# Optimization experiments

Hardware: AMD Instinct MI355X
Metric: run time of the kernel (lower is better)

Reference implementation:

```python
import jax, jax.numpy as jnp
import numpy as np

B_SZ, SEQ_LEN, STATE_DIM, D_IN, D_OUT, KX = 8, 2048, 1024, 512, 512, 10


def setup_inputs() -> dict:
    key = jax.random.key(0)
    ks = jax.random.split(key, 7)
    inputs = jax.random.normal(ks[0], (B_SZ, SEQ_LEN, D_IN), dtype=jnp.float32)
    h0 = jax.random.normal(ks[1], (STATE_DIM,), dtype=jnp.float32)
    # exponential_decay_init(lam=15): x = clamp(-1/lam * log(1-u), max=1); A = (1-x)*sign
    u = jax.random.uniform(ks[2], (STATE_DIM,), dtype=jnp.float32)
    x = jnp.minimum(-(1.0 / 15.0) * jnp.log1p(-u), 1.0)
    sign = jnp.sign(jax.random.normal(ks[3], (STATE_DIM,), dtype=jnp.float32))
    A = (1.0 - x) * sign
    Bm = jax.random.normal(ks[4], (D_IN, STATE_DIM), dtype=jnp.float32) / D_IN
    C = jax.random.normal(ks[5], (STATE_DIM, D_OUT), dtype=jnp.float32) / STATE_DIM
    M = jax.random.normal(ks[6], (D_OUT, D_IN, KX), dtype=jnp.float32) / D_OUT
    return {"inputs": inputs, "h0": h0, "A": A, "B": Bm, "C": C, "M": M}


def _ar_preds(M, x):
    # Equivalent to einsum('oik,bli->bklo') + per-k roll + triu mask + sum over k:
    # ar[b,l,:] = sum_{i=0}^{k-1, i<=l} M[:,:,i] @ x[b, l-i, :]
    b, l, d_in = x.shape
    kx = M.shape[2]
    ar = jnp.einsum('oi,bli->blo', M[:, :, 0], x)
    for i in range(1, kx):
        x_shift = jnp.pad(x, ((0, 0), (i, 0), (0, 0)))[:, :l]  # shift right, zero-fill
        ar = ar + jnp.einsum('oi,bli->blo', M[:, :, i], x_shift)
    return ar


def reference(inputs, h0, A, B, C, M):
    b, l, d_in = inputs.shape
    state_dim = A.shape[0]
    # Project inputs once: u_t @ B for all t -> [b, l, s]
    uB = jnp.einsum('bli,is->bls', inputs, B)

    def step(h, u_t):
        h = A * h + u_t  # diagonal recurrence
        return h, h

    h_init = jnp.broadcast_to(h0, (b, state_dim))
    _, hs = jax.lax.scan(step, h_init, jnp.swapaxes(uB, 0, 1))  # [l, b, s]
    hs = jnp.swapaxes(hs, 0, 1)  # [b, l, s]
    lds_out = hs @ C  # [b, l, d_out]
    return lds_out + _ar_preds(M, inputs)
```

## Files before the change

### kernel.cpp

```cpp
#include <hip/hip_runtime.h>

#define B_SZ   8
#define SEQ    2048
#define PSEQ   (SEQ+16)
#define SDIM   1024
#define DIN    512
#define DOUT   512
#define KX     10
#define RTOT   (B_SZ*SEQ)
#define LC     64
#define NC     (SEQ/LC)

typedef __attribute__((ext_vector_type(8))) short short8;
typedef __attribute__((ext_vector_type(4))) float f32x4;
typedef __attribute__((ext_vector_type(4))) unsigned short bfx4;

#define OFF_XP   0UL
#define OFF_UB   16973824UL
#define OFF_HS   50528256UL
#define OFF_BT   84082688UL
#define OFF_CT   85131264UL
#define OFF_MT   86179840UL

__device__ __forceinline__ short f2bf(float f) {
  unsigned u = __builtin_bit_cast(unsigned, f);
  u += 0x7fffu + ((u >> 16) & 1u);
  return (short)(u >> 16);
}
__device__ __forceinline__ float bf2f(unsigned short b) {
  return __builtin_bit_cast(float, (unsigned)b << 16);
}

#define GLOAD16(gp, lp) __builtin_amdgcn_global_load_lds( \
    (const __attribute__((address_space(1))) void*)(gp), \
    (__attribute__((address_space(3))) void*)(lp), 16, 0, 0)
#define WAITVM(n) asm volatile("s_waitcnt vmcnt(" #n ")" ::: "memory")
#define LGKM0()   do { asm volatile("s_waitcnt lgkmcnt(0)" ::: "memory"); \
                       __builtin_amdgcn_sched_barrier(0); } while (0)
#define SBAR() __builtin_amdgcn_s_barrier()

struct Frags { short8 a[4][2]; short8 b[4][2]; };

__device__ __forceinline__ void read_frags(Frags& f, const short* la, int aoff,
                                           const short* lb, int lane, int wm, int wn) {
  int lr = lane & 15, h = lane >> 4;
  #pragma unroll
  for (int kk = 0; kk < 2; ++kk) {
    int kslot = kk * 4 + h;
    #pragma unroll
    for (int mi = 0; mi < 4; ++mi) {
      int row = aoff + wm * 64 + mi * 16 + lr;
      f.a[mi][kk] = *reinterpret_cast<const short8*>(la + row * 64 + ((kslot ^ (row & 7)) << 3));
    }
    #pragma unroll
    for (int ni = 0; ni < 4; ++ni) {
      int row = wn * 64 + ni * 16 + lr;
      f.b[ni][kk] = *reinterpret_cast<const short8*>(lb + row * 64 + ((kslot ^ (row & 7)) << 3));
    }
  }
}

__device__ __forceinline__ void mfma_frags(const Frags& f, f32x4 acc[4][4]) {
  #pragma unroll
  for (int kk = 0; kk < 2; ++kk)
    #pragma unroll
    for (int mi = 0; mi < 4; ++mi)
      #pragma unroll
      for (int ni = 0; ni < 4; ++ni)
        acc[mi][ni] = __builtin_amdgcn_mfma_f32_16x16x32_bf16(f.a[mi][kk], f.b[ni][kk], acc[mi][ni], 0, 0, 0);
}

__device__ __forceinline__ void sgb_interleave() {
  #pragma unroll
  for (int i = 0; i < 16; ++i) {
    __builtin_amdgcn_sched_group_barrier(0x008, 2, 0);
    __builtin_amdgcn_sched_group_barrier(0x100, 1, 0);
  }
}

__device__ __forceinline__ void stageA256(const short* __restrict__ g, int ld,
                                          short* l, int tid) {
  int rsub = tid >> 3;
  int slot = (tid & 7) ^ (rsub & 7);
  #pragma unroll
  for (int i = 0; i < 4; ++i) {
    int row = i * 64 + rsub;
    GLOAD16(g + (size_t)row * ld + slot * 8, l + row * 64 + (tid & 7) * 8);
  }
}
__device__ __forceinline__ void stageB128(const short* __restrict__ g, int ld,
                                          short* l, int tid) {
  int rsub = tid >> 3;
  int slot = (tid & 7) ^ (rsub & 7);
  #pragma unroll
  for (int i = 0; i < 2; ++i) {
    int row = i * 64 + rsub;
    GLOAD16(g + (size_t)row * ld + slot * 8, l + row * 64 + (tid & 7) * 8);
  }
}
__device__ __forceinline__ void stageX320(const short* __restrict__ g,
                                          short* l, int tid) {
  int rsub = tid >> 3;
  int slot = (tid & 7) ^ (rsub & 7);
  #pragma unroll
  for (int i = 0; i < 5; ++i) {
    int row = i * 64 + rsub;
    GLOAD16(g + (size_t)row * DIN + slot * 8, l + row * 64 + (tid & 7) * 8);
  }
}

__global__ void k_prep1(const float* __restrict__ x, const float* __restrict__ B,
                        short* __restrict__ Xp, short* __restrict__ Bt) {
  __shared__ float t[32][33];
  int blk = blockIdx.x, tid = threadIdx.x;
  if (blk < 2048) {
    const int NG = RTOT * (DIN / 8);
    const int NPAD = B_SZ * 16 * (DIN / 8);
    for (int g = blk * 256 + tid; g < NG + NPAD; g += 2048 * 256) {
      if (g < NG) {
        int r = g >> 6, c8 = g & 63;
        int b = r >> 11, tt = r & 2047;
        const float4* p = reinterpret_cast<const float4*>(x) + (size_t)g * 2;
        float4 f0 = p[0], f1 = p[1];
        short8 o;
        o[0]=f2bf(f0.x); o[1]=f2bf(f0.y); o[2]=f2bf(f0.z); o[3]=f2bf(f0.w);
        o[4]=f2bf(f1.x); o[5]=f2bf(f1.y); o[6]=f2bf(f1.z); o[7]=f2bf(f1.w);
        *reinterpret_cast<short8*>(Xp + ((size_t)(b * PSEQ + 16 + tt) * DIN + c8 * 8)) = o;
      } else {
        int idx = g - NG;
        int b = idx >> 10, rem = idx & 1023;
        int row16 = rem >> 6, c8 = rem & 63;
        const short8 z = {0,0,0,0,0,0,0,0};
        *reinterpret_cast<short8*>(Xp + ((size_t)(b * PSEQ + row16) * DIN + c8 * 8)) = z;
      }
    }
  } else {
    int idx = blk - 2048;
    int bx = (idx & 31) * 32, by = (idx >> 5) * 32;
    int tx = tid & 31, ty = tid >> 5;
    #pragma unroll
    for (int j = 0; j < 32; j += 8)
      t[ty + j][tx] = B[(size_t)(by + ty + j) * SDIM + (bx + tx)];
    __syncthreads();
    #pragma unroll
    for (int j = 0; j < 32; j += 8)
      Bt[(size_t)(bx + ty + j) * DIN + (by + tx)] = f2bf(t[tx][ty + j]);
  }
}

__global__ void k_scan_h(const short* __restrict__ uB, const float* __restrict__ A,
                         const float* __restrict__ h0, const float* __restrict__ E,
                         short* __restrict__ hs,
                         const float* __restrict__ C, const float* __restrict__ M,
                         short* __restrict__ Ct, short* __restrict__ Mt) {
  __shared__ float t[32][33];
  int blk = blockIdx.x, tid = threadIdx.x;
  if (blk < 256) {
    int b = blk >> 5, c = blk & 31;
    int s0 = tid * 4;
    float a[4], h[4], ap[4];
    #pragma unroll
    for (int j = 0; j < 4; ++j) {
      a[j] = A[s0 + j];
      float p = a[j];
      #pragma unroll
      for (int q = 0; q < 6; ++q) p *= p;
      ap[j] = p;
      h[j] = h0[s0 + j];
    }
    const float* Eb = E + (size_t)b * NC * SDIM + s0;
    for (int c2 = 0; c2 < c; ++c2) {
      float4 ev = *reinterpret_cast<const float4*>(Eb + (size_t)c2 * SDIM);
      h[0] = fmaf(ap[0], h[0], ev.x);
      h[1] = fmaf(ap[1], h[1], ev.y);
      h[2] = fmaf(ap[2], h[2], ev.z);
      h[3] = fmaf(ap[3], h[3], ev.w);
    }
    const short* base = uB + ((size_t)b * SEQ + (size_t)c * LC) * SDIM + s0;
    short* hbase = hs + ((size_t)b * SEQ + (size_t)c * LC) * SDIM + s0;
    for (int tt = 0; tt < LC; ++tt) {
      bfx4 v = *reinterpret_cast<const bfx4*>(base + (size_t)tt * SDIM);
      bfx4 o;
      #pragma unroll
      for (int j = 0; j < 4; ++j) {
        h[j] = fmaf(a[j], h[j], bf2f(v[j]));
        o[j] = (unsigned short)f2bf(h[j]);
      }
      *reinterpret_cast<bfx4*>(hbase + (size_t)tt * SDIM) = o;
    }
  } else if (blk < 768) {
    int idx = blk - 256;
    int bx = (idx & 15) * 32, by = (idx >> 4) * 32;
    int tx = tid & 31, ty = tid >> 5;
    #pragma unroll
    for (int j = 0; j < 32; j += 8)
      t[ty + j][tx] = C[(size_t)(by + ty + j) * DOUT + (bx + tx)];
    __syncthreads();
    #pragma unroll
    for (int j = 0; j < 32; j += 8)
      Ct[(size_t)(bx + ty + j) * SDIM + (by + tx)] = f2bf(t[tx][ty + j]);
  } else {
    int idx = (blk - 768) * 256 + tid;
    if (idx < DOUT * DIN) {
      int o = idx / DIN, i = idx - o * DIN;
      const float* src = M + ((size_t)o * DIN + i) * KX;
      #pragma unroll
      for (int tt = 0; tt < KX; ++tt)
        Mt[((size_t)tt * DOUT + o) * DIN + i] = f2bf(src[tt]);
    }
  }
}

__global__ __launch_bounds__(512, 2) void k_gemm_uB(const short* __restrict__ Xp,
                                                    const short* __restrict__ Bt,
                                                    short* __restrict__ uB,
                                                    const float* __restrict__ Adecay,
                                                    float* __restrict__ E) {
  __shared__ __attribute__((aligned(16))) short lds[73728];
  short* const P0 = lds;
  short* const P1 = lds + 24576;
  short* const P2 = lds + 49152;
  int tid = threadIdx.x, lane = tid & 63, w = tid >> 6;
  int wm = w >> 1, wn = w & 1;
  int bid = blockIdx.x;
  long r0 = (long)(bid & 63) * 256;
  int  c0 = (bid >> 6) * 128;
  int  b  = (int)(r0 >> 11);
  const short* Aa = Xp + (size_t)(r0 + 16 * (b + 1)) * DIN;
  const short* Bb = Bt + (size_t)c0 * DIN;

  const f32x4 z4 = {0.f, 0.f, 0.f, 0.f};
  f32x4 acc[4][4];
  #pragma unroll
  for (int mi = 0; mi < 4; ++mi)
    #pragma unroll
    for (int ni = 0; ni < 4; ++ni) acc[mi][ni] = z4;

  Frags fr[2];

  stageA256(Aa,       DIN, P0, tid);  stageB128(Bb,       DIN, P0 + 16384, tid);
  stageA256(Aa + 64,  DIN, P1, tid);  stageB128(Bb + 64,  DIN, P1 + 16384, tid);
  stageA256(Aa + 128, DIN, P2, tid);  stageB128(Bb + 128, DIN, P2 + 16384, tid);
  WAITVM(6);
  SBAR();
  read_frags(fr[0], P0, 0, P0 + 16384, lane, wm, wn);

  #pragma unroll
  for (int s = 0; s < 8; ++s) {
    __builtin_amdgcn_s_setprio(1);
    mfma_frags(fr[s & 1], acc);
    if (s < 7) {
      const short* nb = ((s + 1) % 3 == 0) ? P0 : ((s + 1) % 3 == 1) ? P1 : P2;
      read_frags(fr[(s + 1) & 1], nb, 0, nb + 16384, lane, wm, wn);
      sgb_interleave();
    }
    __builtin_amdgcn_s_setprio(0);
    if (s < 7) {
      LGKM0();
      SBAR();
      if (s <= 4) {
        short* sp = (s % 3 == 0) ? P0 : (s % 3 == 1) ? P1 : P2;
        stageA256(Aa + (s + 3) * 64, DIN, sp, tid);
        stageB128(Bb + (s + 3) * 64, DIN, sp + 16384, tid);
        WAITVM(6);
      } else {
        WAITVM(0);
      }
      SBAR();
    }
  }

  int h = lane >> 4;
  #pragma unroll
  for (int mi = 0; mi < 4; ++mi)
    #pragma unroll
    for (int ni = 0; ni < 4; ++ni)
      #pragma unroll
      for (int r = 0; r < 4; ++r) {
        long row = r0 + wm * 64 + mi * 16 + h * 4 + r;
        int  col = c0 + wn * 64 + ni * 16 + (lane & 15);
        uB[(size_t)row * SDIM + col] = f2bf(acc[mi][ni][r]);
      }
  int cch = (int)((r0 >> 6) & 31) + wm;
  #pragma unroll
  for (int ni = 0; ni < 4; ++ni) {
    int col = c0 + wn * 64 + ni * 16 + (lane & 15);
    float a  = Adecay[col];
    float a2 = a * a, a3 = a2 * a;
    float A4 = a2 * a2;
    float A16 = A4 * A4; A16 = A16 * A16;
    float P16_2 = A16 * A16, P16_3 = P16_2 * A16;
    float Q4 = (h == 3) ? 1.f : (h == 2) ? A4 : (h == 1) ? A4 * A4 : A4 * A4 * A4;
    float cm0 = fmaf(acc[0][ni][0], a3, fmaf(acc[0][ni][1], a2, fmaf(acc[0][ni][2], a, acc[0][ni][3])));
    float cm1 = fmaf(acc[1][ni][0], a3, fmaf(acc[1][ni][1], a2, fmaf(acc[1][ni][2], a, acc[1][ni][3])));
    float cm2 = fmaf(acc[2][ni][0], a3, fmaf(acc[2][ni][1], a2, fmaf(acc[2][ni][2], a, acc[2][ni][3])));
    float cm3 = fmaf(acc[3][ni][0], a3, fmaf(acc[3][ni][1], a2, fmaf(acc[3][ni][2], a, acc[3][ni][3])));
    float L = fmaf(cm0, P16_3, fmaf(cm1, P16_2, fmaf(cm2, A16, cm3)));
    L *= Q4;
    L += __shfl_xor(L, 16);
    L += __shfl_xor(L, 32);
    if (h == 0) E[((size_t)b * NC + cch) * SDIM + col] = L;
  }
}

__global__ __launch_bounds__(512, 2) void k_gemm_out(const short* __restrict__ hs,
                                                     const short* __restrict__ Xp,
                                                     const short* __restrict__ Ct,
                                                     const short* __restrict__ Mt,
                                                     float* __restrict__ out) {
  __shared__ __attribute__((aligned(16))) short lds[81920];
  short* const P0  = lds;
  short* const P1  = lds + 24576;
  short* const P2  = lds + 49152;
  short* const Xs0 = lds;
  short* const Xs1 = lds + 20480;
  short* const PM0 = lds + 57344;
  short* const PM1 = lds + 65536;
  short* const PM2 = lds + 73728;
  int tid = threadIdx.x, lane = tid & 63, w = tid >> 6;
  int wm = w >> 1, wn = w & 1;
  int bid = blockIdx.x;
  int sw  = (bid & 7) * 32 + (bid >> 3);
  long r0 = (long)(sw & 63) * 256;
  int  c0 = (sw >> 6) * 128;
  int  b  = (int)(r0 >> 11);
  const short* hsA = hs + (size_t)r0 * SDIM;
  const short* CtB = Ct + (size_t)c0 * SDIM;
  const short* Xa  = Xp + (size_t)(r0 + 16 * (b + 1) - 16) * DIN;
  const short* MtB = Mt + (size_t)c0 * DIN;

  const f32x4 z4 = {0.f, 0.f, 0.f, 0.f};
  f32x4 acc[4][4];
  #pragma unroll
  for (int mi = 0; mi < 4; ++mi)
    #pragma unroll
    for (int ni = 0; ni < 4; ++ni) acc[mi][ni] = z4;

  Frags fr[2];

  stageA256(hsA,        SDIM, P0, tid);  stageB128(CtB,        SDIM, P0 + 16384, tid);
  stageA256(hsA + 64,   SDIM, P1, tid);  stageB128(CtB + 64,   SDIM, P1 + 16384, tid);
  stageA256(hsA + 128,  SDIM, P2, tid);  stageB128(CtB + 128,  SDIM, P2 + 16384, tid);
  WAITVM(6);
  SBAR();
  read_frags(fr[0], P0, 0, P0 + 16384, lane, wm, wn);

  #pragma unroll
  for (int s = 0; s < 16; ++s) {
    __builtin_amdgcn_s_setprio(1);
    mfma_frags(fr[s & 1], acc);
    if (s < 15) {
      const short* nb = ((s + 1) % 3 == 0) ? P0 : ((s + 1) % 3 == 1) ? P1 : P2;
      read_frags(fr[(s + 1) & 1], nb, 0, nb + 16384, lane, wm, wn);
    } else {
      read_frags(fr[0], Xs0, 16, PM0, lane, wm, wn);
    }
    sgb_interleave();
    __builtin_amdgcn_s_setprio(0);
    LGKM0();
    SBAR();
    if (s <= 12) {
      short* sp = (s % 3 == 0) ? P0 : (s % 3 == 1) ? P1 : P2;
      stageA256(hsA + (s + 3) * 64, SDIM, sp, tid);
      stageB128(CtB + (s + 3) * 64, SDIM, sp + 16384, tid);
      WAITVM(6);
    } else if (s == 13) {
      stageB128(MtB, DIN, PM0, tid);
      stageB128(MtB + (size_t)DOUT * DIN, DIN, PM1, tid);
      WAITVM(4);
    } else if (s == 14) {
      stageB128(MtB + (size_t)2 * DOUT * DIN, DIN, PM2, tid);
      stageX320(Xa, Xs0, tid);
      WAITVM(0);
    }
    SBAR();
  }

  for (int k0 = 0; k0 < 8; ++k0) {
    int kc = k0 * 64;
    const short* xs = (k0 & 1) ? Xs1 : Xs0;
    short*       xn = (k0 & 1) ? Xs0 : Xs1;
    const short* q0 = (k0 % 3 == 0) ? PM0 : (k0 % 3 == 1) ? PM1 : PM2;
    const short* q1 = (k0 % 3 == 0) ? PM1 : (k0 % 3 == 1) ? PM2 : PM0;
    const short* q2 = (k0 % 3 == 0) ? PM2 : (k0 % 3 == 1) ? PM0 : PM1;
    #pragma unroll
    for (int j = 0; j < KX; ++j) {
      __builtin_amdgcn_s_setprio(1);
      mfma_frags(fr[j & 1], acc);
      bool do_read = (j < 9) || (k0 < 7);
      if (j < 9) {
        const short* mn = ((j + 1) % 3 == 0) ? q0 : ((j + 1) % 3 == 1) ? q1 : q2;
        read_frags(fr[(j + 1) & 1], xs, 15 - j, mn, lane, wm, wn);
      } else if (k0 < 7) {
        read_frags(fr[0], xn, 16, q1, lane, wm, wn);
      }
      if (do_read) sgb_interleave();
      __builtin_amdgcn_s_setprio(0);
      LGKM0();
      SBAR();
      if (j + 3 <= 9) {
        short* mw = (j % 3 == 0) ? (short*)q0 : (j % 3 == 1) ? (short*)q1 : (short*)q2;
        stageB128(MtB + (size_t)(j + 3) * DOUT * DIN + kc, DIN, mw, tid);
      } else if (k0 < 7) {
        short* mw = (j % 3 == 0) ? (short*)q0 : (j % 3 == 1) ? (short*)q1 : (short*)q2;
        stageB128(MtB + (size_t)(j - 7) * DOUT * DIN + kc + 64, DIN, mw, tid);
      }
      if (j == 1 && k0 < 7) stageX320(Xa + kc + 64, xn, tid);
      if (j == 1 || j == 2) {
        if (k0 < 7) { WAITVM(7); } else { WAITVM(2); }
      } else if (j >= 7) {
        if (k0 == 7) { WAITVM(0); } else { WAITVM(2); }
      } else {
        WAITVM(2);
      }
      SBAR();
    }
  }

  #pragma unroll
  for (int mi = 0; mi < 4; ++mi)
    #pragma unroll
    for (int ni = 0; ni < 4; ++ni)
      #pragma unroll
      for (int r = 0; r < 4; ++r) {
        long row = r0 + wm * 64 + mi * 16 + (lane >> 4) * 4 + r;
        int  col = c0 + wn * 64 + ni * 16 + (lane & 15);
        out[(size_t)row * DOUT + col] = acc[mi][ni][r];
      }
}

extern "C" void kernel_launch(void* const* d_in, const int* in_sizes, int n_in,
                              void* d_out, int out_size, void* d_ws, size_t ws_size,
                              hipStream_t stream) {
  (void)in_sizes; (void)n_in; (void)out_size; (void)ws_size;
  const float* x  = (const float*)d_in[0];
  const float* h0 = (const float*)d_in[1];
  const float* A  = (const float*)d_in[2];
  const float* B  = (const float*)d_in[3];
  const float* C  = (const float*)d_in[4];
  const float* M  = (const float*)d_in[5];
  float* out = (float*)d_out;
  char* ws = (char*)d_ws;

  short* Xp  = (short*)(ws + OFF_XP);
  short* uB  = (short*)(ws + OFF_UB);
  short* hsb = (short*)(ws + OFF_HS);
  short* Bt  = (short*)(ws + OFF_BT);
  short* Ct  = (short*)(ws + OFF_CT);
  short* Mt  = (short*)(ws + OFF_MT);
  float* E   = out;

  k_prep1<<<2560, 256, 0, stream>>>(x, B, Xp, Bt);
  k_gemm_uB<<<512, 512, 0, stream>>>(Xp, Bt, uB, A, E);
  k_scan_h<<<1792, 256, 0, stream>>>(uB, A, h0, E, hsb, C, M, Ct, Mt);
  k_gemm_out<<<256, 512, 0, stream>>>(hsb, Xp, Ct, Mt, out);
}
```

Measured before the change: 146.9 us.

## Use 4 waves with 128x64 per-wave tiles in output GEMM kernel

```diff
diff --git a/kernel.cpp b/kernel.cpp
--- a/kernel.cpp
+++ b/kernel.cpp
@@ -98,13 +98,34 @@
     GLOAD16(g + (size_t)row * ld + slot * 8, l + row * 64 + (tid & 7) * 8);
   }
 }
-__device__ __forceinline__ void stageX320(const short* __restrict__ g,
-                                          short* l, int tid) {
+
+__device__ __forceinline__ void stageA256_4(const short* __restrict__ g, int ld,
+                                            short* l, int tid) {
   int rsub = tid >> 3;
   int slot = (tid & 7) ^ (rsub & 7);
   #pragma unroll
-  for (int i = 0; i < 5; ++i) {
-    int row = i * 64 + rsub;
+  for (int i = 0; i < 8; ++i) {
+    int row = i * 32 + rsub;
+    GLOAD16(g + (size_t)row * ld + slot * 8, l + row * 64 + (tid & 7) * 8);
+  }
+}
+__device__ __forceinline__ void stageB128_4(const short* __restrict__ g, int ld,
+                                            short* l, int tid) {
+  int rsub = tid >> 3;
+  int slot = (tid & 7) ^ (rsub & 7);
+  #pragma unroll
+  for (int i = 0; i < 4; ++i) {
+    int row = i * 32 + rsub;
+    GLOAD16(g + (size_t)row * ld + slot * 8, l + row * 64 + (tid & 7) * 8);
+  }
+}
+__device__ __forceinline__ void stageX272_4(const short* __restrict__ g,
+                                            short* l, int tid) {
+  stageA256_4(g, DIN, l, tid);
+  if (tid < 128) {
+    int rsub = tid >> 3;
+    int row = 256 + rsub;
+    int slot = (tid & 7) ^ (row & 7);
     GLOAD16(g + (size_t)row * DIN + slot * 8, l + row * 64 + (tid & 7) * 8);
   }
 }
@@ -303,20 +324,59 @@
   }
 }
 
-__global__ __launch_bounds__(512, 2) void k_gemm_out(const short* __restrict__ hs,
+struct Frags4 { short8 a[8][2]; short8 b[4][2]; };
+
+__device__ __forceinline__ void read_frags4(Frags4& f, const short* la, int aoff,
+                                            const short* lb, int lane, int wm, int wn) {
+  int lr = lane & 15, h = lane >> 4;
+  #pragma unroll
+  for (int kk = 0; kk < 2; ++kk) {
+    int kslot = kk * 4 + h;
+    #pragma unroll
+    for (int mi = 0; mi < 8; ++mi) {
+      int row = aoff + wm * 128 + mi * 16 + lr;
+      f.a[mi][kk] = *reinterpret_cast<const short8*>(la + row * 64 + ((kslot ^ (row & 7)) << 3));
+    }
+    #pragma unroll
+    for (int ni = 0; ni < 4; ++ni) {
+      int row = wn * 64 + ni * 16 + lr;
+      f.b[ni][kk] = *reinterpret_cast<const short8*>(lb + row * 64 + ((kslot ^ (row & 7)) << 3));
+    }
+  }
+}
+
+__device__ __forceinline__ void mfma_frags4(const Frags4& f, f32x4 acc[8][4]) {
+  #pragma unroll
+  for (int kk = 0; kk < 2; ++kk)
+    #pragma unroll
+    for (int mi = 0; mi < 8; ++mi)
+      #pragma unroll
+      for (int ni = 0; ni < 4; ++ni)
+        acc[mi][ni] = __builtin_amdgcn_mfma_f32_16x16x32_bf16(f.a[mi][kk], f.b[ni][kk], acc[mi][ni], 0, 0, 0);
+}
+
+__device__ __forceinline__ void sgb_interleave4() {
+  #pragma unroll
+  for (int i = 0; i < 8; ++i) {
+    __builtin_amdgcn_sched_group_barrier(0x008, 8, 0);
+    __builtin_amdgcn_sched_group_barrier(0x100, 3, 0);
+  }
+}
+
+__global__ __launch_bounds__(256, 1) void k_gemm_out(const short* __restrict__ hs,
                                                      const short* __restrict__ Xp,
                                                      const short* __restrict__ Ct,
                                                      const short* __restrict__ Mt,
                                                      float* __restrict__ out) {
-  __shared__ __attribute__((aligned(16))) short lds[81920];
+  __shared__ __attribute__((aligned(16))) short lds[73728];
   short* const P0  = lds;
   short* const P1  = lds + 24576;
   short* const P2  = lds + 49152;
   short* const Xs0 = lds;
-  short* const Xs1 = lds + 20480;
-  short* const PM0 = lds + 57344;
-  short* const PM1 = lds + 65536;
-  short* const PM2 = lds + 73728;
+  short* const Xs1 = lds + 17408;
+  short* const PM0 = lds + 36864;
+  short* const PM1 = lds + 45056;
+  short* const PM2 = lds + 53248;
   int tid = threadIdx.x, lane = tid & 63, w = tid >> 6;
   int wm = w >> 1, wn = w & 1;
   int bid = blockIdx.x;
@@ -330,47 +390,47 @@
   const short* MtB = Mt + (size_t)c0 * DIN;
 
   const f32x4 z4 = {0.f, 0.f, 0.f, 0.f};
-  f32x4 acc[4][4];
-  #pragma unroll
-  for (int mi = 0; mi < 4; ++mi)
+  f32x4 acc[8][4];
+  #pragma unroll
+  for (int mi = 0; mi < 8; ++mi)
     #pragma unroll
     for (int ni = 0; ni < 4; ++ni) acc[mi][ni] = z4;
 
-  Frags fr[2];
-
-  stageA256(hsA,        SDIM, P0, tid);  stageB128(CtB,        SDIM, P0 + 16384, tid);
-  stageA256(hsA + 64,   SDIM, P1, tid);  stageB128(CtB + 64,   SDIM, P1 + 16384, tid);
-  stageA256(hsA + 128,  SDIM, P2, tid);  stageB128(CtB + 128,  SDIM, P2 + 16384, tid);
-  WAITVM(6);
+  Frags4 fr[2];
+
+  stageA256_4(hsA,       SDIM, P0, tid);  stageB128_4(CtB,       SDIM, P0 + 16384, tid);
+  stageA256_4(hsA + 64,  SDIM, P1, tid);  stageB128_4(CtB + 64,  SDIM, P1 + 16384, tid);
+  stageA256_4(hsA + 128, SDIM, P2, tid);  stageB128_4(CtB + 128, SDIM, P2 + 16384, tid);
+  WAITVM(12);
   SBAR();
-  read_frags(fr[0], P0, 0, P0 + 16384, lane, wm, wn);
+  read_frags4(fr[0], P0, 0, P0 + 16384, lane, wm, wn);
 
   #pragma unroll
   for (int s = 0; s < 16; ++s) {
     __builtin_amdgcn_s_setprio(1);
-    mfma_frags(fr[s & 1], acc);
+    mfma_frags4(fr[s & 1], acc);
     if (s < 15) {
       const short* nb = ((s + 1) % 3 == 0) ? P0 : ((s + 1) % 3 == 1) ? P1 : P2;
-      read_frags(fr[(s + 1) & 1], nb, 0, nb + 16384, lane, wm, wn);
+      read_frags4(fr[(s + 1) & 1], nb, 0, nb + 16384, lane, wm, wn);
     } else {
-      read_frags(fr[0], Xs0, 16, PM0, lane, wm, wn);
-    }
-    sgb_interleave();
+      read_frags4(fr[0], Xs0, 16, PM0, lane, wm, wn);
+    }
+    sgb_interleave4();
     __builtin_amdgcn_s_setprio(0);
     LGKM0();
     SBAR();
     if (s <= 12) {
       short* sp = (s % 3 == 0) ? P0 : (s % 3 == 1) ? P1 : P2;
-      stageA256(hsA + (s + 3) * 64, SDIM, sp, tid);
-      stageB128(CtB + (s + 3) * 64, SDIM, sp + 16384, tid);
-      WAITVM(6);
+      stageA256_4(hsA + (s + 3) * 64, SDIM, sp, tid);
+      stageB128_4(CtB + (s + 3) * 64, SDIM, sp + 16384, tid);
+      WAITVM(12);
     } else if (s == 13) {
-      stageB128(MtB, DIN, PM0, tid);
-      stageB128(MtB + (size_t)DOUT * DIN, DIN, PM1, tid);
-      WAITVM(4);
+      stageB128_4(MtB, DIN, PM0, tid);
+      stageB128_4(MtB + (size_t)DOUT * DIN, DIN, PM1, tid);
+      WAITVM(8);
     } else if (s == 14) {
-      stageB128(MtB + (size_t)2 * DOUT * DIN, DIN, PM2, tid);
-      stageX320(Xa, Xs0, tid);
+      stageB128_4(MtB + (size_t)2 * DOUT * DIN, DIN, PM2, tid);
+      stageX272_4(Xa, Xs0, tid);
       WAITVM(0);
     }
     SBAR();
@@ -386,44 +446,44 @@
     #pragma unroll
     for (int j = 0; j < KX; ++j) {
       __builtin_amdgcn_s_setprio(1);
-      mfma_frags(fr[j & 1], acc);
+      mfma_frags4(fr[j & 1], acc);
       bool do_read = (j < 9) || (k0 < 7);
       if (j < 9) {
         const short* mn = ((j + 1) % 3 == 0) ? q0 : ((j + 1) % 3 == 1) ? q1 : q2;
-        read_frags(fr[(j + 1) & 1], xs, 15 - j, mn, lane, wm, wn);
+        read_frags4(fr[(j + 1) & 1], xs, 15 - j, mn, lane, wm, wn);
       } else if (k0 < 7) {
-        read_frags(fr[0], xn, 16, q1, lane, wm, wn);
-      }
-      if (do_read) sgb_interleave();
+        read_frags4(fr[0], xn, 16, q1, lane, wm, wn);
+      }
+      if (do_read) sgb_interleave4();
       __builtin_amdgcn_s_setprio(0);
       LGKM0();
       SBAR();
       if (j + 3 <= 9) {
         short* mw = (j % 3 == 0) ? (short*)q0 : (j % 3 == 1) ? (short*)q1 : (short*)q2;
-        stageB128(MtB + (size_t)(j + 3) * DOUT * DIN + kc, DIN, mw, tid);
+        stageB128_4(MtB + (size_t)(j + 3) * DOUT * DIN + kc, DIN, mw, tid);
       } else if (k0 < 7) {
         short* mw = (j % 3 == 0) ? (short*)q0 : (j % 3 == 1) ? (short*)q1 : (short*)q2;
-        stageB128(MtB + (size_t)(j - 7) * DOUT * DIN + kc + 64, DIN, mw, tid);
-      }
-      if (j == 1 && k0 < 7) stageX320(Xa + kc + 64, xn, tid);
-      if (j == 1 || j == 2) {
-        if (k0 < 7) { WAITVM(7); } else { WAITVM(2); }
-      } else if (j >= 7) {
-        if (k0 == 7) { WAITVM(0); } else { WAITVM(2); }
+        stageB128_4(MtB + (size_t)(j - 7) * DOUT * DIN + kc + 64, DIN, mw, tid);
+      }
+      if (j == 1 && k0 < 7) stageX272_4(Xa + kc + 64, xn, tid);
+      if ((j == 1 || j == 2) && k0 < 7) {
+        WAITVM(12);
+      } else if (j >= 7 && k0 == 7) {
+        WAITVM(0);
       } else {
-        WAITVM(2);
+        WAITVM(4);
       }
       SBAR();
     }
   }
 
   #pragma unroll
-  for (int mi = 0; mi < 4; ++mi)
+  for (int mi = 0; mi < 8; ++mi)
     #pragma unroll
     for (int ni = 0; ni < 4; ++ni)
       #pragma unroll
       for (int r = 0; r < 4; ++r) {
-        long row = r0 + wm * 64 + mi * 16 + (lane >> 4) * 4 + r;
+        long row = r0 + wm * 128 + mi * 16 + (lane >> 4) * 4 + r;
         int  col = c0 + wn * 64 + ni * 16 + (lane & 15);
         out[(size_t)row * DOUT + col] = acc[mi][ni][r];
       }
@@ -453,5 +513,5 @@
   k_prep1<<<2560, 256, 0, stream>>>(x, B, Xp, Bt);
   k_gemm_uB<<<512, 512, 0, stream>>>(Xp, Bt, uB, A, E);
   k_scan_h<<<1792, 256, 0, stream>>>(uB, A, h0, E, hsb, C, M, Ct, Mt);
-  k_gemm_out<<<256, 512, 0, stream>>>(hsb, Xp, Ct, Mt, out);
-}
+  k_gemm_out<<<256, 256, 0, stream>>>(hsb, Xp, Ct, Mt, out);
+}
```

After: 151.8 us. +3.3%, slower.
